# Performance work log

Hardware: AMD Instinct MI355X
Metric: run time of the kernel (lower is better)

## Reference

```python
import jax, jax.numpy as jnp
import numpy as np

N = 50000   # nodes
E = 800000  # directed edges (self-loops added inside reference)
F_IN, H, C = 128, 96, 32


def setup_inputs() -> dict:
    key = jax.random.key(0)
    ks = jax.random.split(key, 8)
    x = jax.random.normal(ks[0], (N, F_IN), dtype=jnp.float32)
    edge_index = jax.random.randint(ks[1], (2, E), 0, N, dtype=jnp.int64)
    W1 = jax.random.normal(ks[2], (F_IN, H), dtype=jnp.float32) * 0.05
    b1 = jnp.zeros((H,), dtype=jnp.float32)
    W2 = jax.random.normal(ks[3], (H, H), dtype=jnp.float32) * 0.05
    b2 = jnp.zeros((H,), dtype=jnp.float32)
    W3 = jax.random.normal(ks[4], (H, C), dtype=jnp.float32) * 0.05
    b3 = jnp.zeros((C,), dtype=jnp.float32)
    return {"x": x, "edge_index": edge_index, "W1": W1, "b1": b1,
            "W2": W2, "b2": b2, "W3": W3, "b3": b3}


def gcn_conv(x, W, b, src, dst, n):
    """PyG GCNConv: x' = D^{-1/2} (A+I) D^{-1/2} (x W) + b (self-loops in src/dst)."""
    xw = x @ W                                        # [n, out]
    ones = jnp.ones(src.shape[0], dtype=xw.dtype)
    deg = jax.ops.segment_sum(ones, dst, num_segments=n)
    dinv = jnp.where(deg > 0, jax.lax.rsqrt(jnp.maximum(deg, 1.0)), 0.0)
    norm = dinv[src] * dinv[dst]                      # [E+n]
    msg = norm[:, None] * xw[src]                     # gather + scale
    out = jax.ops.segment_sum(msg, dst, num_segments=n)  # scatter-add
    return out + b


def reference(x, edge_index, W1, b1, W2, b2, W3, b3):
    loop = jnp.arange(N, dtype=edge_index.dtype)
    src = jnp.concatenate([edge_index[0], loop])      # add self-loops once
    dst = jnp.concatenate([edge_index[1], loop])
    h = jax.nn.relu(gcn_conv(x, W1, b1, src, dst, N))   # dropout is identity (eval)
    h = jax.nn.relu(gcn_conv(h, W2, b2, src, dst, N))
    h = gcn_conv(h, W3, b3, src, dst, N)
    return jax.nn.log_softmax(h, axis=1)
```

## Files before the change

### kernel.cpp

```cpp
#include <hip/hip_runtime.h>
#include <hip/hip_fp16.h>


typedef _Float16 half8 __attribute__((ext_vector_type(8)));
typedef float f32x4 __attribute__((ext_vector_type(4)));
typedef float f32x2 __attribute__((ext_vector_type(2)));

constexpr int CAP = 64;
constexpr int NPB = 128;
constexpr int NBINS_P = 512;
constexpr int EPB = 2048;
constexpr int BCAP = 2560;

__device__ inline __half2 h2u(unsigned int u) {
    union { unsigned int x; __half2 h; } c;
    c.x = u;
    return c.h;
}
__device__ inline unsigned int u_h2(__half2 h) {
    union { __half2 h; unsigned int x; } c;
    c.h = h;
    return c.x;
}

__device__ inline unsigned char f_to_fp8(float f) {
#if __has_builtin(__builtin_amdgcn_cvt_pk_fp8_f32)
    return (unsigned char)(__builtin_amdgcn_cvt_pk_fp8_f32(f, f, 0, false) & 0xFF);
#else
    f = fminf(fmaxf(f, -448.0f), 448.0f);
    unsigned short u = __half_as_ushort(__float2half(f * 0.00390625f));
    unsigned short mag = (unsigned short)((u & 0x7FFF) + 0x40);
    return (unsigned char)(((u >> 8) & 0x80) | (mag >> 7));
#endif
}

__device__ inline float4 fp8x4_to_f4(unsigned int w) {
#if __has_builtin(__builtin_amdgcn_cvt_pk_f32_fp8)
    f32x2 lo = __builtin_amdgcn_cvt_pk_f32_fp8(w, false);
    f32x2 hi = __builtin_amdgcn_cvt_pk_f32_fp8(w, true);
    return {lo[0], lo[1], hi[0], hi[1]};
#else
    unsigned int lo = ((w << 7) & 0x3F80u) | ((w << 8) & 0x8000u);
    unsigned int hi = ((w >> 1) & 0x3F80u) | (w & 0x8000u);
    union { unsigned int u; __half2 h; } cv;
    cv.u = lo | (hi << 16);
    float2 a = __half22float2(cv.h);
    unsigned int lo2 = ((w >> 9) & 0x3F80u) | ((w >> 8) & 0x8000u);
    unsigned int hi2 = ((w >> 17) & 0x3F80u) | ((w >> 16) & 0x8000u);
    cv.u = lo2 | (hi2 << 16);
    float2 b = __half22float2(cv.h);
    return {a.x * 256.f, a.y * 256.f, b.x * 256.f, b.y * 256.f};
#endif
}

__global__ __launch_bounds__(256) void prep_kernel(const int* __restrict__ ei, int twoE,
                                                   int* __restrict__ flags,
                                                   int* __restrict__ bin_cnt,
                                                   const float* __restrict__ W1,
                                                   const float* __restrict__ W2,
                                                   const float* __restrict__ W3,
                                                   __half* __restrict__ Wt1,
                                                   __half* __restrict__ Wt2,
                                                   __half* __restrict__ Wt3) {
    if (blockIdx.x == 0) {
        if (threadIdx.x < 8) flags[threadIdx.x] = 0;
        for (int b = threadIdx.x; b < NBINS_P; b += 256) bin_cnt[b] = 0;
        __syncthreads();
        int c = 0;
        for (int j = threadIdx.x; j < 2048 && j < twoE; j += 256) {
            if ((j & 1) && ei[j] != 0) c++;
        }
        if (c) atomicAdd(&flags[4], c);
        return;
    }
    int i = (blockIdx.x - 1) * 256 + threadIdx.x;
    if (i < 128 * 96) {
        int f = i / 128, k = i - f * 128;
        Wt1[i] = __float2half(W1[(size_t)k * 96 + f]);
    } else if (i < 128 * 96 + 96 * 96) {
        int j = i - 128 * 96;
        int f = j / 96, k = j - f * 96;
        Wt2[j] = __float2half(W2[(size_t)k * 96 + f]);
    } else if (i < 128 * 96 + 96 * 96 + 96 * 32) {
        int j = i - 128 * 96 - 96 * 96;
        int f = j / 96, k = j - f * 96;
        Wt3[j] = __float2half(W3[(size_t)k * 32 + f]);
    }
}

__device__ inline int ld_src(const int* ei, int i, int E, bool i64) {
    if (i64) { int2 v = ((const int2*)ei)[(size_t)i]; return v.x; }
    return ei[i];
}
__device__ inline int ld_dst(const int* ei, int i, int E, bool i64) {
    if (i64) { int2 v = ((const int2*)ei)[(size_t)E + i]; return v.x; }
    return ei[(size_t)E + i];
}

__global__ __launch_bounds__(256) void part_kernel(const int* __restrict__ ei,
                                                   const int* __restrict__ flags,
                                                   int* __restrict__ bin_cnt,
                                                   int* __restrict__ bins, int E, int n) {
    __shared__ int hist[NBINS_P], excl[NBINS_P], cur[NBINS_P], gpos[NBINS_P];
    __shared__ int tmp[256];
    __shared__ int stage[EPB];
    const int tid = threadIdx.x;
    const bool i64 = (flags[4] == 0);
    for (int b = tid; b < NBINS_P; b += 256) hist[b] = 0;
    __syncthreads();

    int v[EPB / 256];
    const int base = blockIdx.x * EPB;
#pragma unroll
    for (int j = 0; j < EPB / 256; j++) {
        int i = base + j * 256 + tid;
        v[j] = -1;
        if (i < E) {
            int s = ld_src(ei, i, E, i64);
            int d = ld_dst(ei, i, E, i64);
            if ((unsigned)s < (unsigned)n && (unsigned)d < (unsigned)n) {
                int bin = d >> 7, ln = d & 127;
                v[j] = (bin << 23) | (ln << 16) | s;
                atomicAdd(&hist[bin], 1);
            }
        }
    }
    __syncthreads();
    int a0 = hist[2 * tid], a1 = hist[2 * tid + 1];
    int pairsum = a0 + a1;
    tmp[tid] = pairsum;
    __syncthreads();
    for (int off = 1; off < 256; off <<= 1) {
        int t = (tid >= off) ? tmp[tid - off] : 0;
        __syncthreads();
        tmp[tid] += t;
        __syncthreads();
    }
    int S = tmp[tid] - pairsum;
    excl[2 * tid] = S;
    excl[2 * tid + 1] = S + a0;
    cur[2 * tid] = S;
    cur[2 * tid + 1] = S + a0;
    __syncthreads();
    for (int b = tid; b < NBINS_P; b += 256)
        gpos[b] = hist[b] ? atomicAdd(&bin_cnt[b], hist[b]) : 0;
#pragma unroll
    for (int j = 0; j < EPB / 256; j++) {
        if (v[j] != -1) {
            int bin = ((unsigned)v[j]) >> 23;
            int p = atomicAdd(&cur[bin], 1);
            stage[p] = v[j];
        }
    }
    __syncthreads();
    int total = excl[NBINS_P - 1] + hist[NBINS_P - 1];
    for (int i = tid; i < total; i += 256) {
        int w = stage[i];
        int bin = ((unsigned)w) >> 23;
        int k = gpos[bin] + (i - excl[bin]);
        if (k < BCAP) bins[(size_t)bin * BCAP + k] = w;
    }
}

__global__ __launch_bounds__(256) void build_kernel(const int* __restrict__ bin_cnt,
                                                    const int* __restrict__ bins,
                                                    int* __restrict__ cnt,
                                                    unsigned short* __restrict__ csr, int n) {
    __shared__ unsigned short lcsr[NPB * CAP];
    __shared__ int lcnt[NPB];
    const int b = blockIdx.x, tid = threadIdx.x;
    for (int i = tid; i < NPB; i += 256) lcnt[i] = 0;
    __syncthreads();
    int m = min(bin_cnt[b], BCAP);
    for (int i = tid; i < m; i += 256) {
        int w = bins[(size_t)b * BCAP + i];
        int ln = (w >> 16) & 127;
        int p = atomicAdd(&lcnt[ln], 1);
        if (p < CAP) lcsr[ln * CAP + p] = (unsigned short)(w & 0xFFFF);
    }
    __syncthreads();
    const int node0 = b * NPB;
    const unsigned int* l32 = (const unsigned int*)lcsr;
    unsigned int* c32 = (unsigned int*)(csr + (size_t)node0 * CAP);
    for (int i = tid; i < NPB * CAP / 2; i += 256) {
        int node = node0 + (i >> 5);
        if (node < n) c32[i] = l32[i];
    }
    for (int t = tid; t < NPB; t += 256)
        if (node0 + t < n) cnt[node0 + t] = lcnt[t];
}

__device__ inline half8 to_h8(float4 u0, float4 u1) {
    half8 r;
    r[0] = (_Float16)u0.x; r[1] = (_Float16)u0.y; r[2] = (_Float16)u0.z; r[3] = (_Float16)u0.w;
    r[4] = (_Float16)u1.x; r[5] = (_Float16)u1.y; r[6] = (_Float16)u1.z; r[7] = (_Float16)u1.w;
    return r;
}

template <int K, int F, bool XF32, bool OUT8>
__global__ __launch_bounds__(256) void gemm_mfma(const void* __restrict__ X,
                                                 const __half* __restrict__ Wt,
                                                 const int* __restrict__ cnt,
                                                 void* __restrict__ out, int n) {
    constexpr int KP = K + 8;
    constexpr int FT = F / 16;
    constexpr int KC = K / 32;
    __shared__ _Float16 Wl[F * KP];
    for (int i = threadIdx.x; i < F * (K / 8); i += 256) {
        int f = i / (K / 8), c = i - f * (K / 8);
        *(half8*)&Wl[f * KP + c * 8] = *(const half8*)&Wt[(size_t)f * K + c * 8];
    }
    __syncthreads();
    const int wave = threadIdx.x >> 6, lane = threadIdx.x & 63;
    const int node0 = (blockIdx.x * 4 + wave) * 16;
    if (node0 >= n) return;
    const int m = lane & 15, q = lane >> 4;
    const int arow = min(node0 + m, n - 1);

    half8 af[KC];
    if (XF32) {
        const float* xp = (const float*)X + (size_t)arow * K + q * 8;
#pragma unroll
        for (int kc = 0; kc < KC; kc++) {
            float4 u0 = *(const float4*)(xp + kc * 32);
            float4 u1 = *(const float4*)(xp + kc * 32 + 4);
            af[kc] = to_h8(u0, u1);
        }
    } else {
        const __half* xp = (const __half*)X + (size_t)arow * K + q * 8;
#pragma unroll
        for (int kc = 0; kc < KC; kc++) af[kc] = *(const half8*)(xp + kc * 32);
    }

    float dv[4];
#pragma unroll
    for (int r = 0; r < 4; r++) {
        int node = node0 + q * 4 + r;
        dv[r] = (node < n) ? rsqrtf(1.0f + (float)cnt[node]) : 0.f;
    }

    f32x4 acc[FT];
#pragma unroll
    for (int t = 0; t < FT; t++) acc[t] = (f32x4)0.f;
#pragma unroll
    for (int kc = 0; kc < KC; kc++) {
#pragma unroll
        for (int t = 0; t < FT; t++) {
            half8 b = *(const half8*)&Wl[(t * 16 + m) * KP + kc * 32 + q * 8];
            acc[t] = __builtin_amdgcn_mfma_f32_16x16x32_f16(af[kc], b, acc[t], 0, 0, 0);
        }
    }
#pragma unroll
    for (int t = 0; t < FT; t++)
#pragma unroll
        for (int r = 0; r < 4; r++) {
            int node = node0 + q * 4 + r;
            if (node < n) {
                float vv = acc[t][r] * dv[r];
                if (OUT8)
                    ((unsigned char*)out)[(size_t)node * F + t * 16 + m] = f_to_fp8(vv);
                else
                    ((__half*)out)[(size_t)node * F + t * 16 + m] = __float2half(vv);
            }
        }
}

__global__ __launch_bounds__(256) void agg96_fp8(const unsigned char* __restrict__ xws,
                                                 const int* __restrict__ cnt,
                                                 const unsigned short* __restrict__ csr,
                                                 const float* __restrict__ bias,
                                                 __half* __restrict__ out, int n) {
    int node = blockIdx.x * 4 + (threadIdx.x >> 6);
    int lane = threadIdx.x & 63;
    if (node >= n) return;
    const int g = lane < 24 ? 0 : 1;
    const int c = g ? lane - 24 : lane;
    const bool act = lane < 48;
    int deg = cnt[node];
    float4 bb = {0.f, 0.f, 0.f, 0.f};
    float4 a = {0.f, 0.f, 0.f, 0.f};
    if (lane < 24) {
        bb = *(const float4*)&bias[c * 4];
        unsigned int w = *(const unsigned int*)(xws + (size_t)node * 96 + c * 4);
        a = fp8x4_to_f4(w);
    }
    int m = min(deg, CAP);
    float dv = rsqrtf(1.0f + (float)deg);
    const uint4* r4 = (const uint4*)(csr + (size_t)node * CAP);
    const unsigned int* r2 = (const unsigned int*)r4;
    int e = 0;
#define G96_U(pr_) (g ? ((pr_) >> 16) : ((pr_) & 0xFFFFu))
#define G96_LD(u_) (*(const unsigned int*)(xws + (size_t)(u_) * 96 + c * 4))
#define G96_ACC(w_) { float4 f_ = fp8x4_to_f4(w_); \
                      a.x += f_.x; a.y += f_.y; a.z += f_.z; a.w += f_.w; }
    for (; e + 16 <= m; e += 16) {
        uint4 pa = r4[e >> 3], pb = r4[(e >> 3) + 1];
        if (act) {
            unsigned int w0 = G96_LD(G96_U(pa.x)), w1 = G96_LD(G96_U(pa.y));
            unsigned int w2 = G96_LD(G96_U(pa.z)), w3 = G96_LD(G96_U(pa.w));
            unsigned int w4 = G96_LD(G96_U(pb.x)), w5 = G96_LD(G96_U(pb.y));
            unsigned int w6 = G96_LD(G96_U(pb.z)), w7 = G96_LD(G96_U(pb.w));
            G96_ACC(w0) G96_ACC(w1) G96_ACC(w2) G96_ACC(w3)
            G96_ACC(w4) G96_ACC(w5) G96_ACC(w6) G96_ACC(w7)
        }
    }
    if (e + 8 <= m) {
        uint4 pa = r4[e >> 3];
        if (act) {
            unsigned int w0 = G96_LD(G96_U(pa.x)), w1 = G96_LD(G96_U(pa.y));
            unsigned int w2 = G96_LD(G96_U(pa.z)), w3 = G96_LD(G96_U(pa.w));
            G96_ACC(w0) G96_ACC(w1) G96_ACC(w2) G96_ACC(w3)
        }
        e += 8;
    }
    if (e + 4 <= m) {
        unsigned int p0 = r2[e >> 1], p1 = r2[(e >> 1) + 1];
        if (act) {
            unsigned int w0 = G96_LD(G96_U(p0)), w1 = G96_LD(G96_U(p1));
            G96_ACC(w0) G96_ACC(w1)
        }
        e += 4;
    }
    if (e + 2 <= m) {
        unsigned int p0 = r2[e >> 1];
        if (act) {
            unsigned int w0 = G96_LD(G96_U(p0));
            G96_ACC(w0)
        }
        e += 2;
    }
    if (e < m && lane < 24) {
        int u = ((const unsigned short*)r4)[e];
        G96_ACC(G96_LD(u))
    }
#undef G96_U
#undef G96_LD
#undef G96_ACC
    float px = __shfl(a.x, lane + 24);
    float py = __shfl(a.y, lane + 24);
    float pz = __shfl(a.z, lane + 24);
    float pw = __shfl(a.w, lane + 24);
    if (lane < 24) {
        a.x += px; a.y += py; a.z += pz; a.w += pw;
        float r0 = fmaxf(fmaf(dv, a.x, bb.x), 0.f);
        float r1 = fmaxf(fmaf(dv, a.y, bb.y), 0.f);
        float r2v = fmaxf(fmaf(dv, a.z, bb.z), 0.f);
        float r3 = fmaxf(fmaf(dv, a.w, bb.w), 0.f);
        union { __half2 h[2]; uint2 u; } pk;
        pk.h[0] = __floats2half2_rn(r0, r1);
        pk.h[1] = __floats2half2_rn(r2v, r3);
        *(uint2*)(out + (size_t)node * 96 + c * 4) = pk.u;
    }
}

__device__ inline int ext8(uint4 p, int j) {
    unsigned int h = (j & 4) ? ((j & 2) ? p.w : p.z) : ((j & 2) ? p.y : p.x);
    return (j & 1) ? (int)(h >> 16) : (int)(h & 0xFFFFu);
}

__global__ __launch_bounds__(256) void agg32_lsm(const __half* __restrict__ xws,
                                                 const int* __restrict__ cnt,
                                                 const unsigned short* __restrict__ csr,
                                                 const float* __restrict__ bias,
                                                 float* __restrict__ out, int n) {
    int node = blockIdx.x * 4 + (threadIdx.x >> 6);
    int lane = threadIdx.x & 63;
    if (node >= n) return;
    const int g = lane >> 4, l = lane & 15;
    int deg = cnt[node];
    float2 b2 = {0.f, 0.f};
    __half2 a = h2u(0u);
    if (g == 0) {
        b2 = *(const float2*)&bias[l * 2];
        a = *(const __half2*)(xws + (size_t)node * 32 + l * 2);
    }
    int m = min(deg, CAP);
    float dv = rsqrtf(1.0f + (float)deg);
    const uint4* r4 = (const uint4*)(csr + (size_t)node * CAP);
    int e = 0;
    for (; e + 16 <= m; e += 16) {
        uint4 pa = r4[e >> 3], pb = r4[(e >> 3) + 1];
        int u0 = ext8(pa, g), u1 = ext8(pa, g + 4);
        int u2 = ext8(pb, g), u3 = ext8(pb, g + 4);
        __half2 f0 = *(const __half2*)(xws + (size_t)u0 * 32 + l * 2);
        __half2 f1 = *(const __half2*)(xws + (size_t)u1 * 32 + l * 2);
        __half2 f2 = *(const __half2*)(xws + (size_t)u2 * 32 + l * 2);
        __half2 f3 = *(const __half2*)(xws + (size_t)u3 * 32 + l * 2);
        a = __hadd2(a, __hadd2(__hadd2(f0, f1), __hadd2(f2, f3)));
    }
    if (e + 8 <= m) {
        uint4 pa = r4[e >> 3];
        int u0 = ext8(pa, g), u1 = ext8(pa, g + 4);
        __half2 f0 = *(const __half2*)(xws + (size_t)u0 * 32 + l * 2);
        __half2 f1 = *(const __half2*)(xws + (size_t)u1 * 32 + l * 2);
        a = __hadd2(a, __hadd2(f0, f1));
        e += 8;
    }
    if (e + 4 <= m) {
        unsigned int p0 = ((const unsigned int*)r4)[e >> 1];
        unsigned int p1 = ((const unsigned int*)r4)[(e >> 1) + 1];
        unsigned int h = (g & 2) ? p1 : p0;
        int u = (g & 1) ? (int)(h >> 16) : (int)(h & 0xFFFF);
        a = __hadd2(a, *(const __half2*)(xws + (size_t)u * 32 + l * 2));
        e += 4;
    }
    for (; e < m; e++) {
        if (g == 0) {
            int u = ((const unsigned short*)r4)[e];
            a = __hadd2(a, *(const __half2*)(xws + (size_t)u * 32 + l * 2));
        }
    }
    a = __hadd2(a, h2u((unsigned int)__shfl_xor((int)u_h2(a), 16)));
    a = __hadd2(a, h2u((unsigned int)__shfl_xor((int)u_h2(a), 32)));
    if (g == 0) {
        float2 av = __half22float2(a);
        float rx = fmaf(dv, av.x, b2.x), ry = fmaf(dv, av.y, b2.y);
        float mx = fmaxf(rx, ry);
        mx = fmaxf(mx, __shfl_xor(mx, 1));
        mx = fmaxf(mx, __shfl_xor(mx, 2));
        mx = fmaxf(mx, __shfl_xor(mx, 4));
        mx = fmaxf(mx, __shfl_xor(mx, 8));
        float s = expf(rx - mx) + expf(ry - mx);
        s += __shfl_xor(s, 1);
        s += __shfl_xor(s, 2);
        s += __shfl_xor(s, 4);
        s += __shfl_xor(s, 8);
        float ls = logf(s);
        ((float2*)out)[(size_t)node * 16 + l] = {rx - mx - ls, ry - mx - ls};
    }
}

extern "C" void kernel_launch(void* const* d_in, const int* in_sizes, int n_in,
                              void* d_out, int out_size, void* d_ws, size_t ws_size,
                              hipStream_t stream) {
    const float* x  = (const float*)d_in[0];
    const int*   ei = (const int*)d_in[1];
    const float* W1 = (const float*)d_in[2];
    const float* b1 = (const float*)d_in[3];
    const float* W2 = (const float*)d_in[4];
    const float* b2 = (const float*)d_in[5];
    const float* W3 = (const float*)d_in[6];
    const float* b3 = (const float*)d_in[7];
    float* out = (float*)d_out;

    const int N_ = in_sizes[0] / 128;
    const int E_ = in_sizes[1] / 2;
    const int NBINS = (N_ + NPB - 1) / NPB;

    char* base = (char*)d_ws;
    size_t off = 0;
    auto take = [&](size_t bytes) {
        void* p = base + off;
        off = (off + bytes + 255) & ~(size_t)255;
        return p;
    };
    int*    flags   = (int*)take(4 * 8);
    int*    bin_cnt = (int*)take(4 * NBINS_P);
    int*    bins    = (int*)take(4 * (size_t)NBINS * BCAP);
    int*    cnt     = (int*)take(4 * (size_t)N_);
    unsigned short* csr = (unsigned short*)take(2 * (size_t)N_ * CAP);
    __half* Wt1     = (__half*)take(2 * 128 * 96);
    __half* Wt2     = (__half*)take(2 * 96 * 96);
    __half* Wt3     = (__half*)take(2 * 96 * 32);
    unsigned char* bufA = (unsigned char*)take(2 * (size_t)N_ * 96);
    __half* bufB    = (__half*)take(2 * (size_t)N_ * 96);

    const int prepBlocks = 1 + (128 * 96 + 96 * 96 + 96 * 32 + 255) / 256;
    prep_kernel<<<prepBlocks, 256, 0, stream>>>(ei, in_sizes[1], flags, bin_cnt,
                                                W1, W2, W3, Wt1, Wt2, Wt3);
    part_kernel<<<(E_ + EPB - 1) / EPB, 256, 0, stream>>>(ei, flags, bin_cnt, bins, E_, N_);
    build_kernel<<<NBINS, 256, 0, stream>>>(bin_cnt, bins, cnt, csr, N_);

    const int gGemm = (N_ + 63) / 64;
    const int gAgg  = (N_ + 3) / 4;

    gemm_mfma<128, 96, true, true><<<gGemm, 256, 0, stream>>>(x, Wt1, cnt, bufA, N_);
    agg96_fp8<<<gAgg, 256, 0, stream>>>(bufA, cnt, csr, b1, bufB, N_);
    gemm_mfma<96, 96, false, true><<<gGemm, 256, 0, stream>>>(bufB, Wt2, cnt, bufA, N_);
    agg96_fp8<<<gAgg, 256, 0, stream>>>(bufA, cnt, csr, b2, bufB, N_);
    gemm_mfma<96, 32, false, false><<<gGemm, 256, 0, stream>>>(bufB, Wt3, cnt, bufA, N_);
    agg32_lsm<<<gAgg, 256, 0, stream>>>((const __half*)bufA, cnt, csr, b3, out, N_);
}
```

Measured before the change: 205.8 us.

## Widen per-lane gathers and increase edge parallelism in 96- and 32-wide aggregation kernels

The 96-wide aggregation now uses 5 groups of 12 lanes, each loading 8 fp8 features (uint2), instead of 2 groups of 24 lanes loading 4 bytes. Neighbour indices are prefetched into registers up front, followed by a multi-step shuffle reduction. The 32-wide log-softmax aggregation switches from 4 groups of 16 lanes with half2 loads to 8 groups of 8 lanes with uint2 loads, so more edges are in flight per wave. The aim is more memory-level parallelism per wave, at the cost of more shuffle reductions and predicated dummy loads for inactive lanes.

```diff
diff --git a/kernel.cpp b/kernel.cpp
--- a/kernel.cpp
+++ b/kernel.cpp
@@ -273,89 +273,92 @@
     int node = blockIdx.x * 4 + (threadIdx.x >> 6);
     int lane = threadIdx.x & 63;
     if (node >= n) return;
-    const int g = lane < 24 ? 0 : 1;
-    const int c = g ? lane - 24 : lane;
-    const bool act = lane < 48;
+    const bool act0 = lane < 60;
+    const int grp = act0 ? lane / 12 : 0;
+    const int c = act0 ? lane - grp * 12 : 0;
     int deg = cnt[node];
-    float4 bb = {0.f, 0.f, 0.f, 0.f};
-    float4 a = {0.f, 0.f, 0.f, 0.f};
-    if (lane < 24) {
-        bb = *(const float4*)&bias[c * 4];
-        unsigned int w = *(const unsigned int*)(xws + (size_t)node * 96 + c * 4);
-        a = fp8x4_to_f4(w);
-    }
     int m = min(deg, CAP);
     float dv = rsqrtf(1.0f + (float)deg);
-    const uint4* r4 = (const uint4*)(csr + (size_t)node * CAP);
-    const unsigned int* r2 = (const unsigned int*)r4;
-    int e = 0;
-#define G96_U(pr_) (g ? ((pr_) >> 16) : ((pr_) & 0xFFFFu))
-#define G96_LD(u_) (*(const unsigned int*)(xws + (size_t)(u_) * 96 + c * 4))
-#define G96_ACC(w_) { float4 f_ = fp8x4_to_f4(w_); \
-                      a.x += f_.x; a.y += f_.y; a.z += f_.z; a.w += f_.w; }
-    for (; e + 16 <= m; e += 16) {
-        uint4 pa = r4[e >> 3], pb = r4[(e >> 3) + 1];
-        if (act) {
-            unsigned int w0 = G96_LD(G96_U(pa.x)), w1 = G96_LD(G96_U(pa.y));
-            unsigned int w2 = G96_LD(G96_U(pa.z)), w3 = G96_LD(G96_U(pa.w));
-            unsigned int w4 = G96_LD(G96_U(pb.x)), w5 = G96_LD(G96_U(pb.y));
-            unsigned int w6 = G96_LD(G96_U(pb.z)), w7 = G96_LD(G96_U(pb.w));
-            G96_ACC(w0) G96_ACC(w1) G96_ACC(w2) G96_ACC(w3)
-            G96_ACC(w4) G96_ACC(w5) G96_ACC(w6) G96_ACC(w7)
-        }
-    }
-    if (e + 8 <= m) {
-        uint4 pa = r4[e >> 3];
-        if (act) {
-            unsigned int w0 = G96_LD(G96_U(pa.x)), w1 = G96_LD(G96_U(pa.y));
-            unsigned int w2 = G96_LD(G96_U(pa.z)), w3 = G96_LD(G96_U(pa.w));
-            G96_ACC(w0) G96_ACC(w1) G96_ACC(w2) G96_ACC(w3)
-        }
-        e += 8;
-    }
-    if (e + 4 <= m) {
-        unsigned int p0 = r2[e >> 1], p1 = r2[(e >> 1) + 1];
-        if (act) {
-            unsigned int w0 = G96_LD(G96_U(p0)), w1 = G96_LD(G96_U(p1));
-            G96_ACC(w0) G96_ACC(w1)
-        }
-        e += 4;
-    }
-    if (e + 2 <= m) {
-        unsigned int p0 = r2[e >> 1];
-        if (act) {
-            unsigned int w0 = G96_LD(G96_U(p0));
-            G96_ACC(w0)
-        }
-        e += 2;
-    }
-    if (e < m && lane < 24) {
-        int u = ((const unsigned short*)r4)[e];
-        G96_ACC(G96_LD(u))
-    }
-#undef G96_U
-#undef G96_LD
-#undef G96_ACC
-    float px = __shfl(a.x, lane + 24);
-    float py = __shfl(a.y, lane + 24);
-    float pz = __shfl(a.z, lane + 24);
-    float pw = __shfl(a.w, lane + 24);
-    if (lane < 24) {
-        a.x += px; a.y += py; a.z += pz; a.w += pw;
-        float r0 = fmaxf(fmaf(dv, a.x, bb.x), 0.f);
-        float r1 = fmaxf(fmaf(dv, a.y, bb.y), 0.f);
-        float r2v = fmaxf(fmaf(dv, a.z, bb.z), 0.f);
-        float r3 = fmaxf(fmaf(dv, a.w, bb.w), 0.f);
-        union { __half2 h[2]; uint2 u; } pk;
+    const unsigned short* row = csr + (size_t)node * CAP;
+    int id[7];
+#pragma unroll
+    for (int i = 0; i < 7; i++) id[i] = row[i * 5 + grp];
+    float4 bb0 = {0.f, 0.f, 0.f, 0.f}, bb1 = {0.f, 0.f, 0.f, 0.f};
+    float4 a0 = {0.f, 0.f, 0.f, 0.f}, a1 = {0.f, 0.f, 0.f, 0.f};
+    if (lane < 12) {
+        bb0 = *(const float4*)&bias[c * 8];
+        bb1 = *(const float4*)&bias[c * 8 + 4];
+        uint2 w = *(const uint2*)(xws + (size_t)node * 96 + c * 8);
+        a0 = fp8x4_to_f4(w.x);
+        a1 = fp8x4_to_f4(w.y);
+    }
+#define A96_ACC(wx_, wy_) { float4 f0_ = fp8x4_to_f4(wx_), f1_ = fp8x4_to_f4(wy_); \
+    a0.x += f0_.x; a0.y += f0_.y; a0.z += f0_.z; a0.w += f0_.w;                    \
+    a1.x += f1_.x; a1.y += f1_.y; a1.z += f1_.z; a1.w += f1_.w; }
+#pragma unroll
+    for (int i = 0; i < 7; i++) {
+        if (m > i * 5) {
+            bool act = act0 && (i * 5 + grp) < m;
+            int u = act ? id[i] : node;
+            uint2 w = *(const uint2*)(xws + (size_t)u * 96 + c * 8);
+            unsigned int wx = act ? w.x : 0u;
+            unsigned int wy = act ? w.y : 0u;
+            A96_ACC(wx, wy)
+        }
+    }
+    for (int e = 35; e < m; e += 5) {
+        bool act = act0 && (e + grp) < m;
+        int u = node;
+        if (act) u = row[e + grp];
+        uint2 w = *(const uint2*)(xws + (size_t)u * 96 + c * 8);
+        unsigned int wx = act ? w.x : 0u;
+        unsigned int wy = act ? w.y : 0u;
+        A96_ACC(wx, wy)
+    }
+#undef A96_ACC
+    {
+        float r;
+        r = __shfl(a0.x, lane + 24); if (lane < 24) a0.x += r;
+        r = __shfl(a0.y, lane + 24); if (lane < 24) a0.y += r;
+        r = __shfl(a0.z, lane + 24); if (lane < 24) a0.z += r;
+        r = __shfl(a0.w, lane + 24); if (lane < 24) a0.w += r;
+        r = __shfl(a1.x, lane + 24); if (lane < 24) a1.x += r;
+        r = __shfl(a1.y, lane + 24); if (lane < 24) a1.y += r;
+        r = __shfl(a1.z, lane + 24); if (lane < 24) a1.z += r;
+        r = __shfl(a1.w, lane + 24); if (lane < 24) a1.w += r;
+        r = __shfl(a0.x, lane + 12); if (lane < 12) a0.x += r;
+        r = __shfl(a0.y, lane + 12); if (lane < 12) a0.y += r;
+        r = __shfl(a0.z, lane + 12); if (lane < 12) a0.z += r;
+        r = __shfl(a0.w, lane + 12); if (lane < 12) a0.w += r;
+        r = __shfl(a1.x, lane + 12); if (lane < 12) a1.x += r;
+        r = __shfl(a1.y, lane + 12); if (lane < 12) a1.y += r;
+        r = __shfl(a1.z, lane + 12); if (lane < 12) a1.z += r;
+        r = __shfl(a1.w, lane + 12); if (lane < 12) a1.w += r;
+        r = __shfl(a0.x, lane + 48); if (lane < 12) a0.x += r;
+        r = __shfl(a0.y, lane + 48); if (lane < 12) a0.y += r;
+        r = __shfl(a0.z, lane + 48); if (lane < 12) a0.z += r;
+        r = __shfl(a0.w, lane + 48); if (lane < 12) a0.w += r;
+        r = __shfl(a1.x, lane + 48); if (lane < 12) a1.x += r;
+        r = __shfl(a1.y, lane + 48); if (lane < 12) a1.y += r;
+        r = __shfl(a1.z, lane + 48); if (lane < 12) a1.z += r;
+        r = __shfl(a1.w, lane + 48); if (lane < 12) a1.w += r;
+    }
+    if (lane < 12) {
+        float r0 = fmaxf(fmaf(dv, a0.x, bb0.x), 0.f);
+        float r1 = fmaxf(fmaf(dv, a0.y, bb0.y), 0.f);
+        float r2 = fmaxf(fmaf(dv, a0.z, bb0.z), 0.f);
+        float r3 = fmaxf(fmaf(dv, a0.w, bb0.w), 0.f);
+        float r4 = fmaxf(fmaf(dv, a1.x, bb1.x), 0.f);
+        float r5 = fmaxf(fmaf(dv, a1.y, bb1.y), 0.f);
+        float r6 = fmaxf(fmaf(dv, a1.z, bb1.z), 0.f);
+        float r7 = fmaxf(fmaf(dv, a1.w, bb1.w), 0.f);
+        union { __half2 h[4]; uint4 u; } pk;
         pk.h[0] = __floats2half2_rn(r0, r1);
-        pk.h[1] = __floats2half2_rn(r2v, r3);
-        *(uint2*)(out + (size_t)node * 96 + c * 4) = pk.u;
-    }
-}
-
-__device__ inline int ext8(uint4 p, int j) {
-    unsigned int h = (j & 4) ? ((j & 2) ? p.w : p.z) : ((j & 2) ? p.y : p.x);
-    return (j & 1) ? (int)(h >> 16) : (int)(h & 0xFFFFu);
+        pk.h[1] = __floats2half2_rn(r2, r3);
+        pk.h[2] = __floats2half2_rn(r4, r5);
+        pk.h[3] = __floats2half2_rn(r6, r7);
+        *(uint4*)(out + (size_t)node * 96 + c * 8) = pk.u;
+    }
 }
 
 __global__ __launch_bounds__(256) void agg32_lsm(const __half* __restrict__ xws,
@@ -366,67 +369,62 @@
     int node = blockIdx.x * 4 + (threadIdx.x >> 6);
     int lane = threadIdx.x & 63;
     if (node >= n) return;
-    const int g = lane >> 4, l = lane & 15;
+    const int g = lane >> 3, c = lane & 7;
     int deg = cnt[node];
-    float2 b2 = {0.f, 0.f};
-    __half2 a = h2u(0u);
-    if (g == 0) {
-        b2 = *(const float2*)&bias[l * 2];
-        a = *(const __half2*)(xws + (size_t)node * 32 + l * 2);
-    }
     int m = min(deg, CAP);
     float dv = rsqrtf(1.0f + (float)deg);
-    const uint4* r4 = (const uint4*)(csr + (size_t)node * CAP);
-    int e = 0;
-    for (; e + 16 <= m; e += 16) {
-        uint4 pa = r4[e >> 3], pb = r4[(e >> 3) + 1];
-        int u0 = ext8(pa, g), u1 = ext8(pa, g + 4);
-        int u2 = ext8(pb, g), u3 = ext8(pb, g + 4);
-        __half2 f0 = *(const __half2*)(xws + (size_t)u0 * 32 + l * 2);
-        __half2 f1 = *(const __half2*)(xws + (size_t)u1 * 32 + l * 2);
-        __half2 f2 = *(const __half2*)(xws + (size_t)u2 * 32 + l * 2);
-        __half2 f3 = *(const __half2*)(xws + (size_t)u3 * 32 + l * 2);
-        a = __hadd2(a, __hadd2(__hadd2(f0, f1), __hadd2(f2, f3)));
-    }
-    if (e + 8 <= m) {
-        uint4 pa = r4[e >> 3];
-        int u0 = ext8(pa, g), u1 = ext8(pa, g + 4);
-        __half2 f0 = *(const __half2*)(xws + (size_t)u0 * 32 + l * 2);
-        __half2 f1 = *(const __half2*)(xws + (size_t)u1 * 32 + l * 2);
-        a = __hadd2(a, __hadd2(f0, f1));
-        e += 8;
-    }
-    if (e + 4 <= m) {
-        unsigned int p0 = ((const unsigned int*)r4)[e >> 1];
-        unsigned int p1 = ((const unsigned int*)r4)[(e >> 1) + 1];
-        unsigned int h = (g & 2) ? p1 : p0;
-        int u = (g & 1) ? (int)(h >> 16) : (int)(h & 0xFFFF);
-        a = __hadd2(a, *(const __half2*)(xws + (size_t)u * 32 + l * 2));
-        e += 4;
-    }
-    for (; e < m; e++) {
-        if (g == 0) {
-            int u = ((const unsigned short*)r4)[e];
-            a = __hadd2(a, *(const __half2*)(xws + (size_t)u * 32 + l * 2));
-        }
-    }
-    a = __hadd2(a, h2u((unsigned int)__shfl_xor((int)u_h2(a), 16)));
-    a = __hadd2(a, h2u((unsigned int)__shfl_xor((int)u_h2(a), 32)));
+    const unsigned short* row = csr + (size_t)node * CAP;
+    int id[4];
+#pragma unroll
+    for (int i = 0; i < 4; i++) id[i] = row[i * 8 + g];
+    float2 b0 = {0.f, 0.f}, b1 = {0.f, 0.f};
+    __half2 a0 = h2u(0u), a1 = h2u(0u);
     if (g == 0) {
-        float2 av = __half22float2(a);
-        float rx = fmaf(dv, av.x, b2.x), ry = fmaf(dv, av.y, b2.y);
-        float mx = fmaxf(rx, ry);
+        b0 = *(const float2*)&bias[c * 4];
+        b1 = *(const float2*)&bias[c * 4 + 2];
+        uint2 s = *(const uint2*)(xws + (size_t)node * 32 + c * 4);
+        a0 = h2u(s.x);
+        a1 = h2u(s.y);
+    }
+#pragma unroll
+    for (int i = 0; i < 4; i++) {
+        if (m > i * 8) {
+            bool act = (i * 8 + g) < m;
+            int u = act ? id[i] : node;
+            uint2 w = *(const uint2*)(xws + (size_t)u * 32 + c * 4);
+            a0 = __hadd2(a0, h2u(act ? w.x : 0u));
+            a1 = __hadd2(a1, h2u(act ? w.y : 0u));
+        }
+    }
+    for (int e = 32; e < m; e += 8) {
+        bool act = (e + g) < m;
+        int u = act ? row[e + g] : node;
+        uint2 w = *(const uint2*)(xws + (size_t)u * 32 + c * 4);
+        a0 = __hadd2(a0, h2u(act ? w.x : 0u));
+        a1 = __hadd2(a1, h2u(act ? w.y : 0u));
+    }
+    a0 = __hadd2(a0, h2u((unsigned int)__shfl_xor((int)u_h2(a0), 32)));
+    a1 = __hadd2(a1, h2u((unsigned int)__shfl_xor((int)u_h2(a1), 32)));
+    a0 = __hadd2(a0, h2u((unsigned int)__shfl_xor((int)u_h2(a0), 16)));
+    a1 = __hadd2(a1, h2u((unsigned int)__shfl_xor((int)u_h2(a1), 16)));
+    a0 = __hadd2(a0, h2u((unsigned int)__shfl_xor((int)u_h2(a0), 8)));
+    a1 = __hadd2(a1, h2u((unsigned int)__shfl_xor((int)u_h2(a1), 8)));
+    if (g == 0) {
+        float2 av0 = __half22float2(a0);
+        float2 av1 = __half22float2(a1);
+        float r0 = fmaf(dv, av0.x, b0.x), r1 = fmaf(dv, av0.y, b0.y);
+        float r2 = fmaf(dv, av1.x, b1.x), r3 = fmaf(dv, av1.y, b1.y);
+        float mx = fmaxf(fmaxf(r0, r1), fmaxf(r2, r3));
         mx = fmaxf(mx, __shfl_xor(mx, 1));
         mx = fmaxf(mx, __shfl_xor(mx, 2));
         mx = fmaxf(mx, __shfl_xor(mx, 4));
-        mx = fmaxf(mx, __shfl_xor(mx, 8));
-        float s = expf(rx - mx) + expf(ry - mx);
+        float s = expf(r0 - mx) + expf(r1 - mx) + expf(r2 - mx) + expf(r3 - mx);
         s += __shfl_xor(s, 1);
         s += __shfl_xor(s, 2);
         s += __shfl_xor(s, 4);
-        s += __shfl_xor(s, 8);
         float ls = logf(s);
-        ((float2*)out)[(size_t)node * 16 + l] = {rx - mx - ls, ry - mx - ls};
+        float4 o = {r0 - mx - ls, r1 - mx - ls, r2 - mx - ls, r3 - mx - ls};
+        ((float4*)out)[(size_t)node * 8 + c] = o;
     }
 }
 
```

Result: no change. 204.5 us, median of 2 (-0.6%).
